# Performance work log

Hardware: AMD Instinct MI355X
Metric: run time of the kernel (lower is better)

Reference implementation:

```python
import jax, jax.numpy as jnp
import numpy as np

B, T, I, H, A, V, OOV = 256, 1, 256, 512, 400, 50000, 50


def _xavier(k, shape):
    fan_out, fan_in = shape[0], shape[-1]
    std = (2.0 / (fan_in + fan_out)) ** 0.5
    return jax.random.normal(k, shape, jnp.float32) * std


def setup_inputs() -> dict:
    key = jax.random.key(0)
    ks = jax.random.split(key, 24)
    return {
        "x": jax.random.normal(ks[0], (B, T, I), jnp.float32),
        "y": jax.random.randint(ks[1], (B, T), 0, V),  # teacher-forcing arg, unused in forward
        "encoder_outputs": jax.random.normal(ks[2], (B, A, A), jnp.float32),
        "encoder_cell": jax.random.normal(ks[3], (B, H), jnp.float32),  # encoder_in[1], unused
        "encoder_state": jax.random.normal(ks[4], (B, H), jnp.float32),
        "max_oov_nums": OOV,
        "ids": jax.random.randint(ks[5], (B, A), 0, V + OOV),
        # LSTM params (PyTorch layout: gates ordered i, f, g, o)
        "W_ih": jax.random.normal(ks[6], (4 * H, I), jnp.float32) * (1.0 / np.sqrt(H)),
        "W_hh": jax.random.normal(ks[7], (4 * H, H), jnp.float32) * (1.0 / np.sqrt(H)),
        "b_ih": jnp.zeros((4 * H,), jnp.float32),
        "b_hh": jnp.zeros((4 * H,), jnp.float32),
        # attention
        "Wh_w": _xavier(ks[8], (A, H)), "Wh_b": jnp.zeros((A,), jnp.float32),
        "Ws_w": _xavier(ks[9], (A, H)), "Ws_b": jnp.zeros((A,), jnp.float32),
        "v": jax.random.normal(ks[10], (A,), jnp.float32),
        # vocab head
        "fc1_w": _xavier(ks[11], (2 * H, H + A)), "fc1_b": jnp.zeros((2 * H,), jnp.float32),
        "fc2_w": _xavier(ks[12], (V, 2 * H)), "fc2_b": jnp.zeros((V,), jnp.float32),
        # p_gen gates (no bias)
        "pg1_w": _xavier(ks[13], (1, I)),
        "pg2_w": _xavier(ks[14], (1, A)),
        "pg3_w": _xavier(ks[15], (1, H)),
    }


def reference(x, y, encoder_outputs, encoder_cell, encoder_state, max_oov_nums, ids,
              W_ih, W_hh, b_ih, b_hh, Wh_w, Wh_b, Ws_w, Ws_b, v,
              fc1_w, fc1_b, fc2_w, fc2_b, pg1_w, pg2_w, pg3_w):
    x0 = x[:, 0, :]  # [B, I] single decode step
    # --- single LSTM step with zero initial (h, c) ---
    gates = x0 @ W_ih.T + b_ih + b_hh  # h0 = 0 so W_hh term vanishes
    i_g, f_g, g_g, o_g = jnp.split(gates, 4, axis=-1)
    c = jax.nn.sigmoid(i_g) * jnp.tanh(g_g)  # c0 = 0
    h = jax.nn.sigmoid(o_g) * jnp.tanh(c)    # decoder_state [B, H]
    # --- Bahdanau-style attention (first step: coverage is zeros, w_c has no bias) ---
    e = jnp.tanh(encoder_state @ Wh_w.T + Wh_b + h @ Ws_w.T + Ws_b)  # [B, A]
    attention = v * jax.nn.softmax(e, axis=-1)  # [B, A]
    # --- context vector: weighted sum over encoder outputs ---
    context = jnp.einsum('ba,bae->be', attention, encoder_outputs)  # [B, A]
    # --- vocab distribution ---
    dec_in = jnp.concatenate([context, h], axis=-1)  # [B, A+H]
    p_vocab = jax.nn.softmax((dec_in @ fc1_w.T + fc1_b) @ fc2_w.T + fc2_b, axis=-1)  # [B, V]
    # --- generation probability gate ---
    gen = jax.nn.sigmoid(context @ pg2_w[0] + x0 @ pg1_w[0] + h @ pg3_w[0])  # [B]
    p_vocab = gen[:, None] * p_vocab
    att_copy = (1.0 - gen)[:, None] * attention
    # --- extended vocab + copy scatter-add ---
    p = jnp.concatenate([p_vocab, jnp.zeros((p_vocab.shape[0], max_oov_nums), p_vocab.dtype)], axis=-1)
    rows = jnp.arange(p.shape[0])[:, None]
    p = p.at[rows, ids].add(att_copy)
    return p
```

## Files before the change

### kernel.cpp

```cpp
#include <hip/hip_runtime.h>
#include <hip/hip_bf16.h>
#include <math.h>

#define BB      256
#define I_DIM   256
#define H_DIM   512
#define A_DIM   400
#define V_DIM   50000
#define OOV     50
#define VP      50050
#define FC1_IN  912
#define FC1_OUT 1024
#define FC2_K   1024

typedef unsigned short u16;
typedef unsigned int   u32;
typedef __attribute__((ext_vector_type(8))) short  short8;
typedef __attribute__((ext_vector_type(4))) float  float4_;

__device__ __forceinline__ u16 f2bf(float f) {
    u32 u = __builtin_bit_cast(u32, f);
    u32 r = (u + 0x7FFFu + ((u >> 16) & 1u)) >> 16;
    return (u16)r;
}

__global__ __launch_bounds__(256)
void sgemm32(const float* __restrict__ Am, const float* __restrict__ Wm,
             float* __restrict__ Cm, const float* __restrict__ bias0,
             const float* __restrict__ bias1, int M, int N, int K,
             int accumulate, int act)
{
    __shared__ float As[16][33];
    __shared__ float Bs[16][33];
    int t  = threadIdx.x;
    int tx = t & 15, ty = t >> 4;
    int m0 = blockIdx.y * 32, n0 = blockIdx.x * 32;
    int lm = t >> 3;
    int lk = (t & 7) * 2;
    const float* aptr = Am + (size_t)(m0 + lm) * K + lk;
    const float* wptr = Wm + (size_t)(n0 + lm) * K + lk;
    bool wvalid = (n0 + lm) < N;
    float c00 = 0.f, c01 = 0.f, c10 = 0.f, c11 = 0.f;

    for (int k0 = 0; k0 < K; k0 += 16) {
        float a0 = aptr[0], a1 = aptr[1];
        float w0 = wvalid ? wptr[0] : 0.f;
        float w1 = wvalid ? wptr[1] : 0.f;
        __syncthreads();
        As[lk][lm] = a0;  As[lk + 1][lm] = a1;
        Bs[lk][lm] = w0;  Bs[lk + 1][lm] = w1;
        __syncthreads();
#pragma unroll
        for (int k = 0; k < 16; ++k) {
            float av0 = As[k][ty], av1 = As[k][ty + 16];
            float bv0 = Bs[k][tx], bv1 = Bs[k][tx + 16];
            c00 += av0 * bv0;  c01 += av0 * bv1;
            c10 += av1 * bv0;  c11 += av1 * bv1;
        }
        aptr += 16; wptr += 16;
    }

    int r0 = m0 + ty, r1 = m0 + ty + 16;
    int cc0 = n0 + tx, cc1 = n0 + tx + 16;
    float accv[2][2] = {{c00, c01}, {c10, c11}};
    int rows[2] = {r0, r1};
    int cols[2] = {cc0, cc1};
#pragma unroll
    for (int i = 0; i < 2; ++i)
#pragma unroll
        for (int j = 0; j < 2; ++j) {
            int c = cols[j];
            if (c < N) {
                size_t idx = (size_t)rows[i] * N + c;
                float v = accv[i][j];
                if (accumulate) v += Cm[idx];
                if (bias0) v += bias0[c];
                if (bias1) v += bias1[c];
                if (act == 1) v = tanhf(v);
                Cm[idx] = v;
            }
        }
}

__global__ __launch_bounds__(256)
void lstm_h_kernel(const float* __restrict__ G, float* __restrict__ hbuf,
                   float* __restrict__ dec_in)
{
    int idx = blockIdx.x * 256 + threadIdx.x;
    int b = idx >> 9, j = idx & 511;
    const float* g = G + (size_t)b * 2048;
    float ig = g[j], gg = g[1024 + j], og = g[1536 + j];
    float si = 1.f / (1.f + expf(-ig));
    float so = 1.f / (1.f + expf(-og));
    float c  = si * tanhf(gg);
    float h  = so * tanhf(c);
    hbuf[idx] = h;
    dec_in[(size_t)b * FC1_IN + A_DIM + j] = h;
}

__global__ __launch_bounds__(256)
void att_kernel(const float* __restrict__ e, const float* __restrict__ vvec,
                float* __restrict__ att)
{
    __shared__ float s_ex[A_DIM];
    __shared__ float red[256];
    int b = blockIdx.x, t = threadIdx.x;
    const float* er = e + (size_t)b * A_DIM;
    float local = 0.f;
    for (int a = t; a < A_DIM; a += 256) {
        float ex = expf(er[a]);
        s_ex[a] = ex; local += ex;
    }
    red[t] = local; __syncthreads();
    for (int s = 128; s > 0; s >>= 1) {
        if (t < s) red[t] += red[t + s];
        __syncthreads();
    }
    float inv = 1.f / red[0];
    for (int a = t; a < A_DIM; a += 256)
        att[(size_t)b * A_DIM + a] = vvec[a] * s_ex[a] * inv;
}

__global__ __launch_bounds__(512)
void ctx_gen_kernel(const float* __restrict__ att, const float* __restrict__ enc,
                    const float* __restrict__ x, const float* __restrict__ h,
                    const float* __restrict__ pg1, const float* __restrict__ pg2,
                    const float* __restrict__ pg3,
                    float* __restrict__ dec_in, float* __restrict__ gen)
{
    __shared__ float s_att[A_DIM];
    __shared__ float red[512];
    int b = blockIdx.x, t = threadIdx.x;
    for (int a = t; a < A_DIM; a += 512) s_att[a] = att[(size_t)b * A_DIM + a];
    __syncthreads();
    float acc = 0.f;
    if (t < A_DIM) {
        const float* ep = enc + (size_t)b * (A_DIM * A_DIM) + t;
#pragma unroll 4
        for (int a = 0; a < A_DIM; ++a) acc += s_att[a] * ep[(size_t)a * A_DIM];
        dec_in[(size_t)b * FC1_IN + t] = acc;
    }
    float local = 0.f;
    if (t < A_DIM) local += acc * pg2[t];
    if (t < I_DIM) local += x[(size_t)b * I_DIM + t] * pg1[t];
    local += h[(size_t)b * H_DIM + t] * pg3[t];
    red[t] = local; __syncthreads();
    for (int s = 256; s > 0; s >>= 1) {
        if (t < s) red[t] += red[t + s];
        __syncthreads();
    }
    if (t == 0) gen[b] = 1.f / (1.f + expf(-red[0]));
}

__global__ __launch_bounds__(256)
void cvt_kernel(const float* __restrict__ hid, u16* __restrict__ hb)
{
    int idx = blockIdx.x * 256 + threadIdx.x;
    hb[idx] = f2bf(hid[idx]);
}

__global__ __launch_bounds__(512)
void fc2_kernel(const u16* __restrict__ hb, const float* __restrict__ W,
                const float* __restrict__ bias, float* __restrict__ out,
                float* __restrict__ sums)
{
    __shared__ __align__(16) u16 Ws[2][64][72];
    int t = threadIdx.x;
    int wv = t >> 6, lane = t & 63;
    int lm = lane & 15, lk = lane >> 4;
    int n0 = blockIdx.x * 64;
    int row_base = wv * 32;

    float4_ acc[2][4];
#pragma unroll
    for (int mi = 0; mi < 2; ++mi)
#pragma unroll
        for (int ni = 0; ni < 4; ++ni)
            acc[mi][ni] = (float4_){0.f, 0.f, 0.f, 0.f};

    int sn = t >> 3;
    int sk = (t & 7) * 8;
    bool svalid = (n0 + sn) < V_DIM;
    const float* wsrc = W + (size_t)(n0 + sn) * FC2_K + sk;

    {
        float4_ w0 = (float4_){0.f,0.f,0.f,0.f}, w1 = w0;
        if (svalid) {
            const float4_* p = (const float4_*)wsrc;
            w0 = p[0]; w1 = p[1];
        }
        short8 wb;
#pragma unroll
        for (int i = 0; i < 4; ++i) {
            wb[i]     = (short)f2bf(w0[i]);
            wb[4 + i] = (short)f2bf(w1[i]);
        }
        *(short8*)&Ws[0][sn][sk] = wb;
    }
    __syncthreads();

    for (int kt = 0; kt < FC2_K / 64; ++kt) {
        int cur = kt & 1;
        float4_ w0 = (float4_){0.f,0.f,0.f,0.f}, w1 = w0;
        bool pf = (kt < FC2_K / 64 - 1);
        if (pf && svalid) {
            const float4_* p = (const float4_*)(wsrc + (kt + 1) * 64);
            w0 = p[0]; w1 = p[1];
        }
        short8 af[2][2];
#pragma unroll
        for (int mi = 0; mi < 2; ++mi)
#pragma unroll
            for (int ks = 0; ks < 2; ++ks)
                af[mi][ks] = *(const short8*)(hb + (size_t)(row_base + mi * 16 + lm) * FC2_K
                                              + kt * 64 + ks * 32 + lk * 8);
#pragma unroll
        for (int ks = 0; ks < 2; ++ks) {
            short8 bfr[4];
#pragma unroll
            for (int ni = 0; ni < 4; ++ni)
                bfr[ni] = *(const short8*)&Ws[cur][ni * 16 + lm][ks * 32 + lk * 8];
#pragma unroll
            for (int mi = 0; mi < 2; ++mi)
#pragma unroll
                for (int ni = 0; ni < 4; ++ni)
                    acc[mi][ni] = __builtin_amdgcn_mfma_f32_16x16x32_bf16(
                        af[mi][ks], bfr[ni], acc[mi][ni], 0, 0, 0);
        }
        if (pf) {
            short8 wb;
#pragma unroll
            for (int i = 0; i < 4; ++i) {
                wb[i]     = (short)f2bf(w0[i]);
                wb[4 + i] = (short)f2bf(w1[i]);
            }
            *(short8*)&Ws[cur ^ 1][sn][sk] = wb;
        }
        __syncthreads();
    }

#pragma unroll
    for (int mi = 0; mi < 2; ++mi) {
        int r_base = row_base + mi * 16 + lk * 4;
        float s[4] = {0.f, 0.f, 0.f, 0.f};
#pragma unroll
        for (int ni = 0; ni < 4; ++ni) {
            int col = n0 + ni * 16 + lm;
            if (col < V_DIM) {
                float bcol = bias[col];
                float4_ a = acc[mi][ni];
#pragma unroll
                for (int r = 0; r < 4; ++r) {
                    float ev = expf(a[r] + bcol);
                    out[(size_t)(r_base + r) * VP + col] = ev;
                    s[r] += ev;
                }
            }
        }
#pragma unroll
        for (int off = 1; off < 16; off <<= 1) {
#pragma unroll
            for (int r = 0; r < 4; ++r) s[r] += __shfl_xor(s[r], off);
        }
        if (lm == 0) {
#pragma unroll
            for (int r = 0; r < 4; ++r) atomicAdd(&sums[r_base + r], s[r]);
        }
    }
}

__global__ __launch_bounds__(256)
void rescale_kernel(float* __restrict__ out, const float* __restrict__ gen,
                    const float* __restrict__ sums)
{
    int idx = (blockIdx.x * 256 + threadIdx.x) * 2;
    int b = idx / VP;
    int c = idx - b * VP;
    float2 v = *(float2*)(out + idx);
    float scale = gen[b] / sums[b];
    v.x = (c     < V_DIM) ? v.x * scale : 0.f;
    v.y = (c + 1 < V_DIM) ? v.y * scale : 0.f;
    *(float2*)(out + idx) = v;
}

__global__ __launch_bounds__(256)
void scatter_kernel(const int* __restrict__ ids, const float* __restrict__ att,
                    const float* __restrict__ gen, float* __restrict__ out)
{
    int idx = blockIdx.x * 256 + threadIdx.x;
    int b = idx / A_DIM;
    float val = (1.f - gen[b]) * att[idx];
    atomicAdd(out + (size_t)b * VP + ids[idx], val);
}

extern "C" void kernel_launch(void* const* d_in, const int* in_sizes, int n_in,
                              void* d_out, int out_size, void* d_ws, size_t ws_size,
                              hipStream_t stream)
{
    const float* x         = (const float*)d_in[0];
    const float* enc       = (const float*)d_in[2];
    const float* enc_state = (const float*)d_in[4];
    const int*   ids       = (const int*)  d_in[6];
    const float* W_ih      = (const float*)d_in[7];
    const float* b_ih      = (const float*)d_in[9];
    const float* b_hh      = (const float*)d_in[10];
    const float* Wh_w      = (const float*)d_in[11];
    const float* Wh_b      = (const float*)d_in[12];
    const float* Ws_w      = (const float*)d_in[13];
    const float* Ws_b      = (const float*)d_in[14];
    const float* vvec      = (const float*)d_in[15];
    const float* fc1_w     = (const float*)d_in[16];
    const float* fc1_b     = (const float*)d_in[17];
    const float* fc2_w     = (const float*)d_in[18];
    const float* fc2_b     = (const float*)d_in[19];
    const float* pg1       = (const float*)d_in[20];
    const float* pg2       = (const float*)d_in[21];
    const float* pg3       = (const float*)d_in[22];
    float* out = (float*)d_out;

    float* ws    = (float*)d_ws;
    float* gates = ws;
    float* hbuf  = gates + 256 * 2048;
    float* ebuf  = hbuf  + 256 * 512;
    float* attb  = ebuf  + 256 * 400;
    float* dec   = attb  + 256 * 400;
    float* hid   = dec   + 256 * 912;
    float* genb  = hid   + 256 * 1024;
    float* sums  = genb  + 256;
    u16*   hbf   = (u16*)(sums + 256);

    sgemm32<<<dim3(64, 8), 256, 0, stream>>>(x, W_ih, gates, b_ih, b_hh,
                                             BB, 2048, I_DIM, 0, 0);
    lstm_h_kernel<<<512, 256, 0, stream>>>(gates, hbuf, dec);
    sgemm32<<<dim3(13, 8), 256, 0, stream>>>(enc_state, Wh_w, ebuf, Wh_b, nullptr,
                                             BB, A_DIM, H_DIM, 0, 0);
    sgemm32<<<dim3(13, 8), 256, 0, stream>>>(hbuf, Ws_w, ebuf, Ws_b, nullptr,
                                             BB, A_DIM, H_DIM, 1, 1);
    att_kernel<<<BB, 256, 0, stream>>>(ebuf, vvec, attb);
    ctx_gen_kernel<<<BB, 512, 0, stream>>>(attb, enc, x, hbuf, pg1, pg2, pg3,
                                           dec, genb);
    sgemm32<<<dim3(32, 8), 256, 0, stream>>>(dec, fc1_w, hid, fc1_b, nullptr,
                                             BB, FC1_OUT, FC1_IN, 0, 0);
    cvt_kernel<<<1024, 256, 0, stream>>>(hid, hbf);
    hipMemsetAsync(sums, 0, BB * sizeof(float), stream);
    fc2_kernel<<<782, 512, 0, stream>>>(hbf, fc2_w, fc2_b, out, sums);
    rescale_kernel<<<(BB * VP) / 512, 256, 0, stream>>>(out, genb, sums);
    scatter_kernel<<<(BB * A_DIM) / 256, 256, 0, stream>>>(ids, attb, genb, out);
}
```

Baseline: 710.6 us.

## Deepen fc2 weight prefetch to two tiles ahead with unrolled LDS double buffer

Restructures the fc2 bf16 MFMA main loop so fp32 weight tiles are loaded from global memory two K-tiles ahead into two register sets, and unrolls the loop by two so each LDS buffer index is a compile-time constant. The conversion and LDS store of the next tile now happen before the MFMAs rather than after them. __syncthreads is replaced with an inline waitcnt-lgkm plus s_barrier. The aim is to hide global load latency on the weight stream and cut barrier overhead, at the cost of more registers held for the in-flight prefetch.

```diff
diff --git a/kernel.cpp b/kernel.cpp
--- a/kernel.cpp
+++ b/kernel.cpp
@@ -22,6 +22,16 @@
     u32 u = __builtin_bit_cast(u32, f);
     u32 r = (u + 0x7FFFu + ((u >> 16) & 1u)) >> 16;
     return (u16)r;
+}
+
+__device__ __forceinline__ short8 cvt_pack8(float4_ a, float4_ b) {
+    short8 r;
+#pragma unroll
+    for (int i = 0; i < 4; ++i) {
+        r[i]     = (short)f2bf(a[i]);
+        r[4 + i] = (short)f2bf(b[i]);
+    }
+    return r;
 }
 
 __global__ __launch_bounds__(256)
@@ -183,60 +193,83 @@
     bool svalid = (n0 + sn) < V_DIM;
     const float* wsrc = W + (size_t)(n0 + sn) * FC2_K + sk;
 
+    const u16* a0 = hb + (size_t)(row_base + lm) * FC2_K + lk * 8;
+    const u16* a1 = a0 + (size_t)16 * FC2_K;
+
+    const float4_ z = (float4_){0.f, 0.f, 0.f, 0.f};
+    float4_ pwa0, pwa1;
+    float4_ pwb0, pwb1;
+
     {
-        float4_ w0 = (float4_){0.f,0.f,0.f,0.f}, w1 = w0;
-        if (svalid) {
-            const float4_* p = (const float4_*)wsrc;
-            w0 = p[0]; w1 = p[1];
-        }
-        short8 wb;
-#pragma unroll
-        for (int i = 0; i < 4; ++i) {
-            wb[i]     = (short)f2bf(w0[i]);
-            wb[4 + i] = (short)f2bf(w1[i]);
-        }
-        *(short8*)&Ws[0][sn][sk] = wb;
-    }
-    __syncthreads();
-
-    for (int kt = 0; kt < FC2_K / 64; ++kt) {
-        int cur = kt & 1;
-        float4_ w0 = (float4_){0.f,0.f,0.f,0.f}, w1 = w0;
-        bool pf = (kt < FC2_K / 64 - 1);
-        if (pf && svalid) {
-            const float4_* p = (const float4_*)(wsrc + (kt + 1) * 64);
-            w0 = p[0]; w1 = p[1];
-        }
-        short8 af[2][2];
-#pragma unroll
-        for (int mi = 0; mi < 2; ++mi)
-#pragma unroll
-            for (int ks = 0; ks < 2; ++ks)
-                af[mi][ks] = *(const short8*)(hb + (size_t)(row_base + mi * 16 + lm) * FC2_K
-                                              + kt * 64 + ks * 32 + lk * 8);
-#pragma unroll
-        for (int ks = 0; ks < 2; ++ks) {
-            short8 bfr[4];
-#pragma unroll
-            for (int ni = 0; ni < 4; ++ni)
-                bfr[ni] = *(const short8*)&Ws[cur][ni * 16 + lm][ks * 32 + lk * 8];
-#pragma unroll
-            for (int mi = 0; mi < 2; ++mi)
+        const float4_* p0 = (const float4_*)(wsrc);
+        const float4_* p1 = (const float4_*)(wsrc + 64);
+        pwa0 = svalid ? p0[0] : z;  pwa1 = svalid ? p0[1] : z;
+        pwb0 = svalid ? p1[0] : z;  pwb1 = svalid ? p1[1] : z;
+    }
+    *(short8*)&Ws[0][sn][sk] = cvt_pack8(pwa0, pwa1);
+    asm volatile("s_waitcnt lgkmcnt(0)\n\ts_barrier" ::: "memory");
+
+#pragma unroll 1
+    for (int j = 0; j < 8; ++j) {
+        {
+            int kt = 2 * j;
+            if (j < 7) {
+                const float4_* p = (const float4_*)(wsrc + (kt + 2) * 64);
+                pwa0 = svalid ? p[0] : z;
+                pwa1 = svalid ? p[1] : z;
+            }
+            int kb = kt * 64;
+            short8 af00 = *(const short8*)(a0 + kb);
+            short8 af01 = *(const short8*)(a0 + kb + 32);
+            short8 af10 = *(const short8*)(a1 + kb);
+            short8 af11 = *(const short8*)(a1 + kb + 32);
+            *(short8*)&Ws[1][sn][sk] = cvt_pack8(pwb0, pwb1);
+#pragma unroll
+            for (int ks = 0; ks < 2; ++ks) {
+                short8 bfr[4];
 #pragma unroll
                 for (int ni = 0; ni < 4; ++ni)
-                    acc[mi][ni] = __builtin_amdgcn_mfma_f32_16x16x32_bf16(
-                        af[mi][ks], bfr[ni], acc[mi][ni], 0, 0, 0);
-        }
-        if (pf) {
-            short8 wb;
-#pragma unroll
-            for (int i = 0; i < 4; ++i) {
-                wb[i]     = (short)f2bf(w0[i]);
-                wb[4 + i] = (short)f2bf(w1[i]);
-            }
-            *(short8*)&Ws[cur ^ 1][sn][sk] = wb;
-        }
-        __syncthreads();
+                    bfr[ni] = *(const short8*)&Ws[0][ni * 16 + lm][ks * 32 + lk * 8];
+                short8 afp0 = ks ? af01 : af00;
+                short8 afp1 = ks ? af11 : af10;
+#pragma unroll
+                for (int ni = 0; ni < 4; ++ni) {
+                    acc[0][ni] = __builtin_amdgcn_mfma_f32_16x16x32_bf16(afp0, bfr[ni], acc[0][ni], 0, 0, 0);
+                    acc[1][ni] = __builtin_amdgcn_mfma_f32_16x16x32_bf16(afp1, bfr[ni], acc[1][ni], 0, 0, 0);
+                }
+            }
+            asm volatile("s_waitcnt lgkmcnt(0)\n\ts_barrier" ::: "memory");
+        }
+        {
+            int kt = 2 * j + 1;
+            if (j < 7) {
+                const float4_* p = (const float4_*)(wsrc + (kt + 2) * 64);
+                pwb0 = svalid ? p[0] : z;
+                pwb1 = svalid ? p[1] : z;
+            }
+            int kb = kt * 64;
+            short8 af00 = *(const short8*)(a0 + kb);
+            short8 af01 = *(const short8*)(a0 + kb + 32);
+            short8 af10 = *(const short8*)(a1 + kb);
+            short8 af11 = *(const short8*)(a1 + kb + 32);
+            if (j < 7)
+                *(short8*)&Ws[0][sn][sk] = cvt_pack8(pwa0, pwa1);
+#pragma unroll
+            for (int ks = 0; ks < 2; ++ks) {
+                short8 bfr[4];
+#pragma unroll
+                for (int ni = 0; ni < 4; ++ni)
+                    bfr[ni] = *(const short8*)&Ws[1][ni * 16 + lm][ks * 32 + lk * 8];
+                short8 afp0 = ks ? af01 : af00;
+                short8 afp1 = ks ? af11 : af10;
+#pragma unroll
+                for (int ni = 0; ni < 4; ++ni) {
+                    acc[0][ni] = __builtin_amdgcn_mfma_f32_16x16x32_bf16(afp0, bfr[ni], acc[0][ni], 0, 0, 0);
+                    acc[1][ni] = __builtin_amdgcn_mfma_f32_16x16x32_bf16(afp1, bfr[ni], acc[1][ni], 0, 0, 0);
+                }
+            }
+            asm volatile("s_waitcnt lgkmcnt(0)\n\ts_barrier" ::: "memory");
+        }
     }
 
 #pragma unroll
```

Result: no change. 705.5 us (-0.7%).
